# Kernel optimization log

Measured on AMD Instinct MI355X. Metric: run time of the kernel, lower is better.

The kernel has to match this reference:

```python
import jax, jax.numpy as jnp
import numpy as np

BSZ, SEQ, EMBED = 2, 4096, 1024
NUM_HEADS = 16
HEAD_DIM = EMBED // NUM_HEADS
WINDOW = 256  # attention_window[layer_id]


def setup_inputs() -> dict:
    key = jax.random.key(0)
    ks = jax.random.split(key, 7)
    s = 1.0 / np.sqrt(EMBED)
    return {
        "hidden_states": jax.random.normal(ks[0], (BSZ, SEQ, EMBED), jnp.float32),
        "Wq": jax.random.normal(ks[1], (EMBED, EMBED), jnp.float32) * s,
        "bq": jnp.zeros((EMBED,), jnp.float32),
        "Wk": jax.random.normal(ks[2], (EMBED, EMBED), jnp.float32) * s,
        "bk": jnp.zeros((EMBED,), jnp.float32),
        "Wv": jax.random.normal(ks[3], (EMBED, EMBED), jnp.float32) * s,
        "bv": jnp.zeros((EMBED,), jnp.float32),
    }


def _blocks3(x, nb, w):
    # x: [b, s + 2w, h, d] -> [b, nb, 3w, h, d]; block c sees key blocks c-1, c, c+1
    b = x.shape[0]
    xb = x.reshape(b, nb + 2, w, NUM_HEADS, HEAD_DIM)
    return jnp.concatenate([xb[:, i:i + nb] for i in range(3)], axis=2)


def reference(hidden_states, Wq, bq, Wk, bk, Wv, bv):
    b, s, e = hidden_states.shape
    w = WINDOW
    nb = s // w
    q = (hidden_states @ Wq + bq) * (1.0 / np.sqrt(HEAD_DIM))
    k = hidden_states @ Wk + bk
    v = hidden_states @ Wv + bv
    q = q.reshape(b, nb, w, NUM_HEADS, HEAD_DIM)
    k = k.reshape(b, s, NUM_HEADS, HEAD_DIM)
    v = v.reshape(b, s, NUM_HEADS, HEAD_DIM)
    pad = ((0, 0), (w, w), (0, 0), (0, 0))
    kb = _blocks3(jnp.pad(k, pad), nb, w)  # [b, nb, 3w, h, d]
    vb = _blocks3(jnp.pad(v, pad), nb, w)
    # banded scores: query x in block n attends keys at global pos n*w - w + y
    scores = jnp.einsum('bnxhd,bnyhd->bnhxy', q, kb)  # [b, nb, h, w, 3w]
    x_idx = jnp.arange(w)
    y_idx = jnp.arange(3 * w)
    band = jnp.abs(y_idx[None, :] - x_idx[:, None] - w) <= w  # [w, 3w]
    kpos = jnp.arange(nb)[:, None] * w - w + y_idx[None, :]   # [nb, 3w]
    inb = (kpos >= 0) & (kpos < s)
    mask = band[None, :, :] & inb[:, None, :]                 # [nb, w, 3w]
    scores = jnp.where(mask[None, :, None, :, :], scores, -jnp.inf)
    probs = jax.nn.softmax(scores.astype(jnp.float32), axis=-1).astype(v.dtype)
    attn = jnp.einsum('bnhxy,bnyhd->bnxhd', probs, vb)        # [b, nb, w, h, d]
    return attn.reshape(b, s, e)
```

## Files before the change

### kernel.cpp

```cpp
#include <hip/hip_runtime.h>
#include <stdint.h>

#define SEQ    4096
#define EMBED  1024
#define NHEAD  16
#define HDIM   64
#define WIN    256
#define BSZ    2
#define M_TOT  (BSZ * SEQ)
#define N_QKV  3072
#define N_QK   2048
#define K_DIM  1024
#define LOG2E  1.4426950408889634f

typedef __attribute__((ext_vector_type(8))) __bf16 bf16x8;
typedef __attribute__((ext_vector_type(4))) float  f32x4;

__device__ __forceinline__ unsigned short f2bf(float f) {
  union { float f; unsigned int u; } c; c.f = f;
  unsigned int u = c.u;
  unsigned int r = (u + 0x7FFFu + ((u >> 16) & 1u)) >> 16;
  return (unsigned short)r;
}

__device__ __forceinline__ void gl2lds16(const void* g, void* l) {
  __builtin_amdgcn_global_load_lds((const __attribute__((address_space(1))) void*)g,
                                   (__attribute__((address_space(3))) void*)l, 16, 0, 0);
}

__global__ __launch_bounds__(256) void cvt_h(const float* __restrict__ in,
                                             unsigned short* __restrict__ out) {
  int i = (blockIdx.x * 256 + threadIdx.x) * 4;
  float4 v = *(const float4*)(in + i);
  ushort4 o;
  o.x = f2bf(v.x); o.y = f2bf(v.y); o.z = f2bf(v.z); o.w = f2bf(v.w);
  *(ushort4*)(out + i) = o;
}

__global__ __launch_bounds__(256) void cvt_w(const float* __restrict__ Wq,
                                             const float* __restrict__ Wk,
                                             const float* __restrict__ Wv,
                                             unsigned short* __restrict__ Wt) {
  __shared__ float t[32][33];
  int z = blockIdx.z;
  const float* W = (z == 0) ? Wq : (z == 1) ? Wk : Wv;
  int kb = blockIdx.x * 32, nb = blockIdx.y * 32;
  int tx = threadIdx.x, ty = threadIdx.y;
  for (int it = 0; it < 4; ++it) {
    int k = kb + ty + it * 8;
    t[ty + it * 8][tx] = W[(size_t)k * 1024 + nb + tx];
  }
  __syncthreads();
  for (int it = 0; it < 4; ++it) {
    int n = nb + ty + it * 8;
    Wt[(size_t)(z * 1024 + n) * 1024 + kb + tx] = f2bf(t[tx][ty + it * 8]);
  }
}

__global__ __launch_bounds__(256) void qkv_gemm(const unsigned short* __restrict__ A,
                                                const unsigned short* __restrict__ Bt,
                                                const float* __restrict__ bq,
                                                const float* __restrict__ bk,
                                                const float* __restrict__ bv,
                                                unsigned short* __restrict__ C,
                                                unsigned short* __restrict__ Vt) {
  __shared__ unsigned short As[128 * 32];
  __shared__ unsigned short Bs[128 * 32];
  int tid  = threadIdx.x;
  int lane = tid & 63, wave = tid >> 6;
  int ln   = lane & 15, quad = lane >> 4;
  int m0 = blockIdx.y * 128, n0 = blockIdx.x * 128;
  int wy = wave >> 1, wx = wave & 1;
  f32x4 acc[4][4];
  for (int i = 0; i < 4; ++i)
    for (int j = 0; j < 4; ++j) acc[i][j] = (f32x4){0.f, 0.f, 0.f, 0.f};

  for (int k0 = 0; k0 < K_DIM; k0 += 32) {
    __syncthreads();
    for (int it = 0; it < 2; ++it) {
      int chunk = wave * 128 + it * 64 + lane;
      int row = chunk >> 2, cb = chunk & 3;
      gl2lds16(A + (size_t)(m0 + row) * K_DIM + k0 + cb * 8,
               As + (size_t)(wave * 128 + it * 64) * 8);
    }
    for (int it = 0; it < 2; ++it) {
      int chunk = wave * 128 + it * 64 + lane;
      int row = chunk >> 2, cb = chunk & 3;
      gl2lds16(Bt + (size_t)(n0 + row) * K_DIM + k0 + cb * 8,
               Bs + (size_t)(wave * 128 + it * 64) * 8);
    }
    __syncthreads();
    bf16x8 af[4], bfr[4];
    for (int i = 0; i < 4; ++i)
      af[i] = *(const bf16x8*)&As[(wy * 64 + i * 16 + ln) * 32 + quad * 8];
    for (int j = 0; j < 4; ++j)
      bfr[j] = *(const bf16x8*)&Bs[(wx * 64 + j * 16 + ln) * 32 + quad * 8];
    for (int i = 0; i < 4; ++i)
      for (int j = 0; j < 4; ++j)
        acc[i][j] = __builtin_amdgcn_mfma_f32_16x16x32_bf16(af[i], bfr[j], acc[i][j], 0, 0, 0);
  }

  if (n0 < N_QK) {
    for (int j = 0; j < 4; ++j) {
      int n = n0 + wx * 64 + j * 16 + ln;
      float bias, scl;
      if (n < 1024) { bias = bq[n];        scl = 0.125f * LOG2E; }
      else          { bias = bk[n - 1024]; scl = 1.f; }
      for (int i = 0; i < 4; ++i) {
        int mb = m0 + wy * 64 + i * 16 + quad * 4;
        for (int r = 0; r < 4; ++r) {
          float v = (acc[i][j][r] + bias) * scl;
          C[(size_t)(mb + r) * N_QK + n] = f2bf(v);
        }
      }
    }
  } else {
    for (int j = 0; j < 4; ++j) {
      int n  = n0 + wx * 64 + j * 16 + ln;
      int hd = n - 2048;
      float bias = bv[hd];
      for (int i = 0; i < 4; ++i) {
        int mb  = m0 + wy * 64 + i * 16 + quad * 4;
        int bb  = mb >> 12;
        int pos = mb & (SEQ - 1);
        ushort4 pk;
        pk.x = f2bf(acc[i][j][0] + bias);
        pk.y = f2bf(acc[i][j][1] + bias);
        pk.z = f2bf(acc[i][j][2] + bias);
        pk.w = f2bf(acc[i][j][3] + bias);
        *(ushort4*)&Vt[((size_t)bb * (NHEAD * HDIM) + hd) * SEQ + pos] = pk;
      }
    }
  }
}

__global__ __launch_bounds__(256) void attn(const unsigned short* __restrict__ qk,
                                            const unsigned short* __restrict__ vtg,
                                            float* __restrict__ out) {
  __shared__ unsigned short KV[128 * 72];
  unsigned short* Kl = KV;
  unsigned short* Vl = KV + 64 * 72;
  unsigned short* Pl = KV;
  int tid  = threadIdx.x;
  int lane = tid & 63, wave = tid >> 6;
  int ln   = lane & 15, quad = lane >> 4;
  int q0 = blockIdx.x * 64, head = blockIdx.y, b = blockIdx.z;
  size_t baseRow = (size_t)b * SEQ;
  const unsigned short* kptr = qk + 1024;
  const unsigned short* vrow = vtg + ((size_t)(b * NHEAD + head) * HDIM) * SEQ;

  int sy = tid >> 3, sc = tid & 7;
  const unsigned short* kbase = kptr + (baseRow + sy) * (size_t)N_QK + head * HDIM + sc * 8;
  const unsigned short* vbase = vrow + (size_t)sy * SEQ + sc * 8;

  bf16x8 qf[2];
  {
    size_t ro = (baseRow + q0 + wave * 16 + ln) * (size_t)N_QK + head * HDIM + quad * 8;
    qf[0] = *(const bf16x8*)&qk[ro];
    qf[1] = *(const bf16x8*)&qk[ro + 32];
  }

  float l_st = 0.f;
  f32x4 o_acc[4];
  for (int dt = 0; dt < 4; ++dt) o_acc[dt] = (f32x4){0.f, 0.f, 0.f, 0.f};

  int lo = (q0 >= 256) ? 0 : (256 - q0) / 64;
  int hi = (SEQ + 256 - q0) / 64; if (hi > 9) hi = 9;

  uint4 pk0, pk1, pv0, pv1;
#define PREFETCH(KT)                                                        \
  {                                                                         \
    pk0 = *(const uint4*)&kbase[(size_t)(KT) * N_QK];                       \
    pk1 = *(const uint4*)&kbase[(size_t)((KT) + 32) * N_QK];                \
    pv0 = *(const uint4*)&vbase[(KT) + 32 * SEQ * 0 + (size_t)32 * SEQ * 0];\
    pv0 = *(const uint4*)&vbase[(KT)];                                      \
    pv1 = *(const uint4*)&vbase[(size_t)32 * SEQ + (KT)];                   \
  }

  PREFETCH(q0 - 256 + lo * 64);

  for (int t = lo; t < hi; ++t) {
    int kt = q0 - 256 + t * 64;
    __syncthreads();
    *(uint4*)&Kl[sy * 72 + sc * 8]        = pk0;
    *(uint4*)&Kl[(sy + 32) * 72 + sc * 8] = pk1;
    *(uint4*)&Vl[sy * 72 + sc * 8]        = pv0;
    *(uint4*)&Vl[(sy + 32) * 72 + sc * 8] = pv1;
    __syncthreads();

    if (t + 1 < hi) { PREFETCH(kt + 64); }

    f32x4 s[4];
    for (int nt = 0; nt < 4; ++nt) {
      bf16x8 kf0 = *(const bf16x8*)&Kl[(nt * 16 + ln) * 72 + quad * 8];
      bf16x8 kf1 = *(const bf16x8*)&Kl[(nt * 16 + ln) * 72 + 32 + quad * 8];
      f32x4 z = (f32x4){0.f, 0.f, 0.f, 0.f};
      z = __builtin_amdgcn_mfma_f32_16x16x32_bf16(kf0, qf[0], z, 0, 0, 0);
      z = __builtin_amdgcn_mfma_f32_16x16x32_bf16(kf1, qf[1], z, 0, 0, 0);
      s[nt] = z;
    }

    if (t == 0 || t == 8) {
      int qq = q0 + wave * 16 + ln;
      for (int nt = 0; nt < 4; ++nt) {
        int kb = kt + nt * 16 + quad * 4 - qq;
        for (int r = 0; r < 4; ++r) {
          int dd = kb + r;
          if (dd < -WIN || dd > WIN) s[nt][r] = -INFINITY;
        }
      }
    }

    float rs = 0.f;
    for (int nt = 0; nt < 4; ++nt)
      for (int r = 0; r < 4; ++r) {
        float p = exp2f(s[nt][r]);
        s[nt][r] = p;
        rs += p;
      }
    l_st += rs;

    __syncthreads();
    for (int nt = 0; nt < 4; ++nt) {
      ushort4 pq;
      pq.x = f2bf(s[nt][0]);
      pq.y = f2bf(s[nt][1]);
      pq.z = f2bf(s[nt][2]);
      pq.w = f2bf(s[nt][3]);
      *(ushort4*)&Pl[(wave * 16 + ln) * 72 + nt * 16 + quad * 4] = pq;
    }
    for (int ks = 0; ks < 2; ++ks) {
      bf16x8 pf = *(const bf16x8*)&Pl[(wave * 16 + ln) * 72 + ks * 32 + quad * 8];
      for (int dt = 0; dt < 4; ++dt) {
        bf16x8 vf = *(const bf16x8*)&Vl[(dt * 16 + ln) * 72 + ks * 32 + quad * 8];
        o_acc[dt] = __builtin_amdgcn_mfma_f32_16x16x32_bf16(pf, vf, o_acc[dt], 0, 0, 0);
      }
    }
  }

  float l = l_st;
  l += __shfl_xor(l, 16);
  l += __shfl_xor(l, 32);
  float inv = 1.0f / l;
  float li[4];
  for (int r = 0; r < 4; ++r)
    li[r] = __shfl(inv, (lane & 48) | (quad * 4 + r));
  for (int dt = 0; dt < 4; ++dt)
    for (int r = 0; r < 4; ++r) {
      int qpos = q0 + wave * 16 + quad * 4 + r;
      out[(baseRow + qpos) * (size_t)EMBED + head * HDIM + dt * 16 + ln] =
          o_acc[dt][r] * li[r];
    }
#undef PREFETCH
}

extern "C" void kernel_launch(void* const* d_in, const int* in_sizes, int n_in,
                              void* d_out, int out_size, void* d_ws, size_t ws_size,
                              hipStream_t stream) {
  const float* h  = (const float*)d_in[0];
  const float* Wq = (const float*)d_in[1];
  const float* bq = (const float*)d_in[2];
  const float* Wk = (const float*)d_in[3];
  const float* bk = (const float*)d_in[4];
  const float* Wv = (const float*)d_in[5];
  const float* bv = (const float*)d_in[6];
  float* out = (float*)d_out;

  unsigned short* h_bf  = (unsigned short*)d_ws;
  unsigned short* wt_bf = h_bf + (size_t)M_TOT * K_DIM;
  unsigned short* qk    = wt_bf + (size_t)N_QKV * K_DIM;
  unsigned short* vtg   = qk + (size_t)M_TOT * N_QK;

  cvt_h<<<(M_TOT * K_DIM) / 1024, 256, 0, stream>>>(h, h_bf);
  cvt_w<<<dim3(32, 32, 3), dim3(32, 8), 0, stream>>>(Wq, Wk, Wv, wt_bf);
  qkv_gemm<<<dim3(N_QKV / 128, M_TOT / 128), 256, 0, stream>>>(h_bf, wt_bf, bq, bk, bv, qk, vtg);
  attn<<<dim3(SEQ / 64, NHEAD, BSZ), 256, 0, stream>>>(qk, vtg, out);
}
```

Baseline: 228.5 us.

## Double GEMM K-tile with XOR swizzle; pass attention probs via shuffles

The QKV GEMM now stages 64-wide K tiles with an XOR-swizzled LDS layout, halving the barriers per K sweep and reducing LDS bank conflicts on fragment reads. In the attention kernel, P is no longer written to LDS and read back behind an extra barrier. It is redistributed into MFMA operand layout with cross-lane shuffles, and the MFMA operands are swapped so the output is transposed, which lets each thread store a float4. The trade-offs are a larger LDS footprint for the GEMM, more shuffle instructions, and K and V now held in separate LDS buffers.

```diff
diff --git a/kernel.cpp b/kernel.cpp
--- a/kernel.cpp
+++ b/kernel.cpp
@@ -64,8 +64,8 @@
                                                 const float* __restrict__ bv,
                                                 unsigned short* __restrict__ C,
                                                 unsigned short* __restrict__ Vt) {
-  __shared__ unsigned short As[128 * 32];
-  __shared__ unsigned short Bs[128 * 32];
+  __shared__ unsigned short As[128 * 64];
+  __shared__ unsigned short Bs[128 * 64];
   int tid  = threadIdx.x;
   int lane = tid & 63, wave = tid >> 6;
   int ln   = lane & 15, quad = lane >> 4;
@@ -75,29 +75,37 @@
   for (int i = 0; i < 4; ++i)
     for (int j = 0; j < 4; ++j) acc[i][j] = (f32x4){0.f, 0.f, 0.f, 0.f};
 
-  for (int k0 = 0; k0 < K_DIM; k0 += 32) {
-    __syncthreads();
-    for (int it = 0; it < 2; ++it) {
-      int chunk = wave * 128 + it * 64 + lane;
-      int row = chunk >> 2, cb = chunk & 3;
-      gl2lds16(A + (size_t)(m0 + row) * K_DIM + k0 + cb * 8,
-               As + (size_t)(wave * 128 + it * 64) * 8);
-    }
-    for (int it = 0; it < 2; ++it) {
-      int chunk = wave * 128 + it * 64 + lane;
-      int row = chunk >> 2, cb = chunk & 3;
-      gl2lds16(Bt + (size_t)(n0 + row) * K_DIM + k0 + cb * 8,
-               Bs + (size_t)(wave * 128 + it * 64) * 8);
-    }
-    __syncthreads();
-    bf16x8 af[4], bfr[4];
-    for (int i = 0; i < 4; ++i)
-      af[i] = *(const bf16x8*)&As[(wy * 64 + i * 16 + ln) * 32 + quad * 8];
-    for (int j = 0; j < 4; ++j)
-      bfr[j] = *(const bf16x8*)&Bs[(wx * 64 + j * 16 + ln) * 32 + quad * 8];
-    for (int i = 0; i < 4; ++i)
-      for (int j = 0; j < 4; ++j)
-        acc[i][j] = __builtin_amdgcn_mfma_f32_16x16x32_bf16(af[i], bfr[j], acc[i][j], 0, 0, 0);
+  for (int k0 = 0; k0 < K_DIM; k0 += 64) {
+    __syncthreads();
+    for (int it = 0; it < 4; ++it) {
+      int chunk = it * 256 + wave * 64 + lane;
+      int row = chunk >> 3, c = chunk & 7;
+      int cg = c ^ (row & 7);
+      gl2lds16(A + (size_t)(m0 + row) * K_DIM + k0 + cg * 8, As + chunk * 8);
+    }
+    for (int it = 0; it < 4; ++it) {
+      int chunk = it * 256 + wave * 64 + lane;
+      int row = chunk >> 3, c = chunk & 7;
+      int cg = c ^ (row & 7);
+      gl2lds16(Bt + (size_t)(n0 + row) * K_DIM + k0 + cg * 8, Bs + chunk * 8);
+    }
+    __syncthreads();
+    for (int ks2 = 0; ks2 < 2; ++ks2) {
+      bf16x8 af[4], bfr[4];
+      for (int i = 0; i < 4; ++i) {
+        int row = wy * 64 + i * 16 + ln;
+        int c = (ks2 * 4 + quad) ^ (row & 7);
+        af[i] = *(const bf16x8*)&As[row * 64 + c * 8];
+      }
+      for (int j = 0; j < 4; ++j) {
+        int row = wx * 64 + j * 16 + ln;
+        int c = (ks2 * 4 + quad) ^ (row & 7);
+        bfr[j] = *(const bf16x8*)&Bs[row * 64 + c * 8];
+      }
+      for (int i = 0; i < 4; ++i)
+        for (int j = 0; j < 4; ++j)
+          acc[i][j] = __builtin_amdgcn_mfma_f32_16x16x32_bf16(af[i], bfr[j], acc[i][j], 0, 0, 0);
+    }
   }
 
   if (n0 < N_QK) {
@@ -137,10 +145,8 @@
 __global__ __launch_bounds__(256) void attn(const unsigned short* __restrict__ qk,
                                             const unsigned short* __restrict__ vtg,
                                             float* __restrict__ out) {
-  __shared__ unsigned short KV[128 * 72];
-  unsigned short* Kl = KV;
-  unsigned short* Vl = KV + 64 * 72;
-  unsigned short* Pl = KV;
+  __shared__ unsigned short Kl[64 * 72];
+  __shared__ unsigned short Vl[64 * 72];
   int tid  = threadIdx.x;
   int lane = tid & 63, wave = tid >> 6;
   int ln   = lane & 15, quad = lane >> 4;
@@ -172,12 +178,15 @@
   {                                                                         \
     pk0 = *(const uint4*)&kbase[(size_t)(KT) * N_QK];                       \
     pk1 = *(const uint4*)&kbase[(size_t)((KT) + 32) * N_QK];                \
-    pv0 = *(const uint4*)&vbase[(KT) + 32 * SEQ * 0 + (size_t)32 * SEQ * 0];\
     pv0 = *(const uint4*)&vbase[(KT)];                                      \
     pv1 = *(const uint4*)&vbase[(size_t)32 * SEQ + (KT)];                   \
   }
 
   PREFETCH(q0 - 256 + lo * 64);
+
+  int srcA = ((lane & 16) << 1) | ln;
+  int srcB = srcA + 16;
+  bool hiQ = (lane & 32) != 0;
 
   for (int t = lo; t < hi; ++t) {
     int kt = q0 - 256 + t * 64;
@@ -220,20 +229,30 @@
       }
     l_st += rs;
 
-    __syncthreads();
+    unsigned int p01[4], p23[4];
     for (int nt = 0; nt < 4; ++nt) {
-      ushort4 pq;
-      pq.x = f2bf(s[nt][0]);
-      pq.y = f2bf(s[nt][1]);
-      pq.z = f2bf(s[nt][2]);
-      pq.w = f2bf(s[nt][3]);
-      *(ushort4*)&Pl[(wave * 16 + ln) * 72 + nt * 16 + quad * 4] = pq;
-    }
+      p01[nt] = (unsigned int)f2bf(s[nt][0]) | ((unsigned int)f2bf(s[nt][1]) << 16);
+      p23[nt] = (unsigned int)f2bf(s[nt][2]) | ((unsigned int)f2bf(s[nt][3]) << 16);
+    }
+
     for (int ks = 0; ks < 2; ++ks) {
-      bf16x8 pf = *(const bf16x8*)&Pl[(wave * 16 + ln) * 72 + ks * 32 + quad * 8];
+      int ntA = 2 * ks, ntB = 2 * ks + 1;
+      unsigned int a0 = (unsigned int)__shfl((int)p01[ntA], srcA);
+      unsigned int a1 = (unsigned int)__shfl((int)p23[ntA], srcA);
+      unsigned int a2 = (unsigned int)__shfl((int)p01[ntA], srcB);
+      unsigned int a3 = (unsigned int)__shfl((int)p23[ntA], srcB);
+      unsigned int b0 = (unsigned int)__shfl((int)p01[ntB], srcA);
+      unsigned int b1 = (unsigned int)__shfl((int)p23[ntB], srcA);
+      unsigned int b2 = (unsigned int)__shfl((int)p01[ntB], srcB);
+      unsigned int b3 = (unsigned int)__shfl((int)p23[ntB], srcB);
+      union { uint4 u; bf16x8 v; } pf;
+      pf.u.x = hiQ ? b0 : a0;
+      pf.u.y = hiQ ? b1 : a1;
+      pf.u.z = hiQ ? b2 : a2;
+      pf.u.w = hiQ ? b3 : a3;
       for (int dt = 0; dt < 4; ++dt) {
         bf16x8 vf = *(const bf16x8*)&Vl[(dt * 16 + ln) * 72 + ks * 32 + quad * 8];
-        o_acc[dt] = __builtin_amdgcn_mfma_f32_16x16x32_bf16(pf, vf, o_acc[dt], 0, 0, 0);
+        o_acc[dt] = __builtin_amdgcn_mfma_f32_16x16x32_bf16(vf, pf.v, o_acc[dt], 0, 0, 0);
       }
     }
   }
@@ -242,15 +261,16 @@
   l += __shfl_xor(l, 16);
   l += __shfl_xor(l, 32);
   float inv = 1.0f / l;
-  float li[4];
-  for (int r = 0; r < 4; ++r)
-    li[r] = __shfl(inv, (lane & 48) | (quad * 4 + r));
-  for (int dt = 0; dt < 4; ++dt)
-    for (int r = 0; r < 4; ++r) {
-      int qpos = q0 + wave * 16 + quad * 4 + r;
-      out[(baseRow + qpos) * (size_t)EMBED + head * HDIM + dt * 16 + ln] =
-          o_acc[dt][r] * li[r];
-    }
+  int qpos = q0 + wave * 16 + ln;
+  float* ob = out + (baseRow + qpos) * (size_t)EMBED + head * HDIM + quad * 4;
+  for (int dt = 0; dt < 4; ++dt) {
+    float4 v;
+    v.x = o_acc[dt][0] * inv;
+    v.y = o_acc[dt][1] * inv;
+    v.z = o_acc[dt][2] * inv;
+    v.w = o_acc[dt][3] * inv;
+    *(float4*)(ob + dt * 16) = v;
+  }
 #undef PREFETCH
 }
 
```

Result: no change. 225.5 us (-1.3%).
